# Kernel optimization log

Measured on AMD Instinct MI355X. Metric: run time of the kernel, lower is better.

The kernel has to match this reference:

```python
import jax, jax.numpy as jnp
import numpy as np

D_MODEL = 768
NUM_HEADS = 12
D_K = D_MODEL // NUM_HEADS


def setup_inputs() -> dict:
    key = jax.random.key(0)
    ks = jax.random.split(key, 7)
    B, T = 2, 2048
    scale = 1.0 / np.sqrt(D_MODEL)
    return {
        "query": jax.random.normal(ks[0], (B, T, D_MODEL), dtype=jnp.float32),
        "key": jax.random.normal(ks[1], (B, T, D_MODEL), dtype=jnp.float32),
        "value": jax.random.normal(ks[2], (B, T, D_MODEL), dtype=jnp.float32),
        # nn.Linear(d_model, d_model, bias=False) weights, stored [out, in] as in torch
        "W_q": jax.random.normal(ks[3], (D_MODEL, D_MODEL), dtype=jnp.float32) * scale,
        "W_k": jax.random.normal(ks[4], (D_MODEL, D_MODEL), dtype=jnp.float32) * scale,
        "W_v": jax.random.normal(ks[5], (D_MODEL, D_MODEL), dtype=jnp.float32) * scale,
        "W_o": jax.random.normal(ks[6], (D_MODEL, D_MODEL), dtype=jnp.float32) * scale,
    }


def _split_heads(x):
    # [B, T, H*Dk] -> [B, H, T, Dk]
    B, T, _ = x.shape
    return x.reshape(B, T, NUM_HEADS, D_K).transpose(0, 2, 1, 3)


def reference(query, key, value, W_q, W_k, W_v, W_o):
    # Linear projections (torch Linear: y = x @ W.T)
    Q = _split_heads(query @ W_q.T)
    K = _split_heads(key @ W_k.T)
    V = _split_heads(value @ W_v.T)

    # Naive scaled dot-product attention: full [B,H,Tq,Tk] score matrix
    scores = jnp.einsum("bhqd,bhkd->bhqk", Q, K) / jnp.sqrt(jnp.float32(D_K))
    weights = jax.nn.softmax(scores, axis=-1)
    attn = jnp.einsum("bhqk,bhkd->bhqd", weights, V)

    # [B,H,T,Dk] -> [B,T,D_model], then output projection
    B, H, T, Dk = attn.shape
    attn = attn.transpose(0, 2, 1, 3).reshape(B, T, H * Dk)
    output = attn @ W_o.T
    return output, weights
```

## Files before the change

kernel.cpp:

```cpp
#include <hip/hip_runtime.h>
#include <cstdint>

#define HD   12
#define TSEQ 2048
#define DM   768
#define DK   64
#define BATCH 2
#define NZ   (BATCH * HD)
#define RS_N (NZ * TSEQ)

template<bool SUMA, bool EXPROW>
__device__ __forceinline__ void gemm_nt_core(
    const float* __restrict__ A, const float* __restrict__ A2,
    const float* __restrict__ B, float* __restrict__ C,
    int m0, int n0, int K, int lda, int ldb, int ldc, float alpha,
    float* __restrict__ rowsum, int rowbase)
{
    __shared__ float As[16][132];
    __shared__ float Bs[16][132];

    const int t = threadIdx.x;
    const int row = t & 127;
    const int kh8 = (t >> 7) * 8;
    const float* Arow = A + (size_t)(m0 + row) * lda + kh8;
    const float* Brow = B + (size_t)(n0 + row) * ldb + kh8;
    const float* A2row = nullptr;
    if (SUMA) A2row = A2 + (size_t)(m0 + row) * lda + kh8;

    const int w  = t >> 6;
    const int l  = t & 63;
    const int orow = (w >> 1) * 64 + (l >> 3) * 8;
    const int ocol = (w & 1) * 64 + (l & 7) * 8;

    float acc[8][8];
    #pragma unroll
    for (int i = 0; i < 8; ++i)
        #pragma unroll
        for (int j = 0; j < 8; ++j) acc[i][j] = 0.f;

    float4 a0 = *(const float4*)(Arow);
    float4 a1 = *(const float4*)(Arow + 4);
    float4 b0 = *(const float4*)(Brow);
    float4 b1 = *(const float4*)(Brow + 4);
    float4 c0, c1;
    if (SUMA) { c0 = *(const float4*)(A2row); c1 = *(const float4*)(A2row + 4); }

    for (int k0 = 0; k0 < K; k0 += 16) {
        __syncthreads();
        if (SUMA) {
            a0.x += c0.x; a0.y += c0.y; a0.z += c0.z; a0.w += c0.w;
            a1.x += c1.x; a1.y += c1.y; a1.z += c1.z; a1.w += c1.w;
        }
        As[kh8 + 0][row] = a0.x; As[kh8 + 1][row] = a0.y;
        As[kh8 + 2][row] = a0.z; As[kh8 + 3][row] = a0.w;
        As[kh8 + 4][row] = a1.x; As[kh8 + 5][row] = a1.y;
        As[kh8 + 6][row] = a1.z; As[kh8 + 7][row] = a1.w;
        Bs[kh8 + 0][row] = b0.x; Bs[kh8 + 1][row] = b0.y;
        Bs[kh8 + 2][row] = b0.z; Bs[kh8 + 3][row] = b0.w;
        Bs[kh8 + 4][row] = b1.x; Bs[kh8 + 5][row] = b1.y;
        Bs[kh8 + 6][row] = b1.z; Bs[kh8 + 7][row] = b1.w;
        __syncthreads();
        if (k0 + 16 < K) {
            a0 = *(const float4*)(Arow + k0 + 16);
            a1 = *(const float4*)(Arow + k0 + 20);
            b0 = *(const float4*)(Brow + k0 + 16);
            b1 = *(const float4*)(Brow + k0 + 20);
            if (SUMA) {
                c0 = *(const float4*)(A2row + k0 + 16);
                c1 = *(const float4*)(A2row + k0 + 20);
            }
        }
        #pragma unroll
        for (int kk = 0; kk < 16; ++kk) {
            const float4 f0 = *(const float4*)&As[kk][orow];
            const float4 f1 = *(const float4*)&As[kk][orow + 4];
            const float4 g0 = *(const float4*)&Bs[kk][ocol];
            const float4 g1 = *(const float4*)&Bs[kk][ocol + 4];
            const float a[8] = {f0.x, f0.y, f0.z, f0.w, f1.x, f1.y, f1.z, f1.w};
            const float b[8] = {g0.x, g0.y, g0.z, g0.w, g1.x, g1.y, g1.z, g1.w};
            #pragma unroll
            for (int i = 0; i < 8; ++i)
                #pragma unroll
                for (int j = 0; j < 8; ++j)
                    acc[i][j] = fmaf(a[i], b[j], acc[i][j]);
        }
    }

    if (EXPROW) {
        float rs[8];
        #pragma unroll
        for (int i = 0; i < 8; ++i) {
            rs[i] = 0.f;
            #pragma unroll
            for (int j = 0; j < 8; ++j) {
                acc[i][j] = __expf(acc[i][j] * alpha);
                rs[i] += acc[i][j];
            }
            float* crow = C + (size_t)(m0 + orow + i) * ldc + n0 + ocol;
            *(float4*)crow = make_float4(acc[i][0], acc[i][1], acc[i][2], acc[i][3]);
            *(float4*)(crow + 4) = make_float4(acc[i][4], acc[i][5], acc[i][6], acc[i][7]);
        }
        #pragma unroll
        for (int i = 0; i < 8; ++i) {
            rs[i] += __shfl_xor(rs[i], 1);
            rs[i] += __shfl_xor(rs[i], 2);
            rs[i] += __shfl_xor(rs[i], 4);
        }
        if ((l & 7) == 0) {
            #pragma unroll
            for (int i = 0; i < 8; ++i)
                atomicAdd(&rowsum[rowbase + m0 + orow + i], rs[i]);
        }
    } else {
        #pragma unroll
        for (int i = 0; i < 8; ++i) {
            float* crow = C + (size_t)(m0 + orow + i) * ldc + n0 + ocol;
            *(float4*)crow = make_float4(acc[i][0] * alpha, acc[i][1] * alpha,
                                         acc[i][2] * alpha, acc[i][3] * alpha);
            *(float4*)(crow + 4) = make_float4(acc[i][4] * alpha, acc[i][5] * alpha,
                                               acc[i][6] * alpha, acc[i][7] * alpha);
        }
    }
}

__global__ __launch_bounds__(256) void gemm_qkv(
    const float* __restrict__ q, const float* __restrict__ k,
    const float* __restrict__ v,
    const float* __restrict__ Wq, const float* __restrict__ Wk,
    const float* __restrict__ Wv,
    float* __restrict__ Qp, float* __restrict__ Kp, float* __restrict__ Vp)
{
    const int by  = blockIdx.y;
    const int mat = by / 6;
    const int nb  = by % 6;
    const float* A = (mat == 0) ? q  : (mat == 1) ? k  : v;
    const float* B = (mat == 0) ? Wq : (mat == 1) ? Wk : Wv;
    float*       C = (mat == 0) ? Qp : (mat == 1) ? Kp : Vp;
    gemm_nt_core<false, false>(A, nullptr, B, C, blockIdx.x * 128, nb * 128,
                               DM, DM, DM, DM, 1.f, nullptr, 0);
}

template<bool SUMA>
__global__ __launch_bounds__(256) void gemm_out(
    const float* __restrict__ ctx0, const float* __restrict__ ctx1,
    const float* __restrict__ Wo, float* __restrict__ out)
{
    gemm_nt_core<SUMA, false>(ctx0, ctx1, Wo, out, blockIdx.x * 128,
                              blockIdx.y * 128, DM, DM, DM, DM, 1.f, nullptr, 0);
}

template<bool EXPROW>
__global__ __launch_bounds__(256) void attn_scores(
    const float* __restrict__ Qp, const float* __restrict__ Kp,
    float* __restrict__ Wt, float* __restrict__ rowsum)
{
    const int z = blockIdx.z, b = z / HD, h = z % HD;
    gemm_nt_core<false, EXPROW>(Qp + (size_t)b * TSEQ * DM + h * DK, nullptr,
                                Kp + (size_t)b * TSEQ * DM + h * DK,
                                Wt + (size_t)z * TSEQ * TSEQ,
                                blockIdx.x * 128, blockIdx.y * 128,
                                DK, DM, DM, TSEQ, 0.125f, rowsum, z * TSEQ);
}

__global__ __launch_bounds__(256) void zero_buf(float* __restrict__ p, int n)
{
    const int i = blockIdx.x * 256 + threadIdx.x;
    if (i < n) p[i] = 0.f;
}

__global__ __launch_bounds__(256) void softmax_rows(float* __restrict__ Wt)
{
    float* p = Wt + (size_t)blockIdx.x * TSEQ;
    const int t = threadIdx.x;
    const float4 va = *(const float4*)(p + t * 4);
    const float4 vb = *(const float4*)(p + 1024 + t * 4);
    float v[8] = {va.x, va.y, va.z, va.w, vb.x, vb.y, vb.z, vb.w};

    float m = -3.4e38f;
    #pragma unroll
    for (int i = 0; i < 8; ++i) m = fmaxf(m, v[i]);
    #pragma unroll
    for (int off = 32; off > 0; off >>= 1) m = fmaxf(m, __shfl_down(m, off));
    __shared__ float redm[4];
    __shared__ float reds[4];
    const int lane = t & 63, wid = t >> 6;
    if (lane == 0) redm[wid] = m;
    __syncthreads();
    m = fmaxf(fmaxf(redm[0], redm[1]), fmaxf(redm[2], redm[3]));
    float s = 0.f;
    #pragma unroll
    for (int i = 0; i < 8; ++i) { v[i] = __expf(v[i] - m); s += v[i]; }
    #pragma unroll
    for (int off = 32; off > 0; off >>= 1) s += __shfl_down(s, off);
    if (lane == 0) reds[wid] = s;
    __syncthreads();
    s = reds[0] + reds[1] + reds[2] + reds[3];
    const float inv = 1.f / s;
    *(float4*)(p + t * 4) =
        make_float4(v[0] * inv, v[1] * inv, v[2] * inv, v[3] * inv);
    *(float4*)(p + 1024 + t * 4) =
        make_float4(v[4] * inv, v[5] * inv, v[6] * inv, v[7] * inv);
}

template<bool NORM>
__global__ __launch_bounds__(256) void attn_pv(
    float* __restrict__ Wt, const float* __restrict__ Vp,
    const float* __restrict__ rowsum, float* __restrict__ ctxp, int kchunk)
{
    const int z = blockIdx.z, b = z / HD, h = z % HD;
    const int kbase = blockIdx.y * kchunk;
    float* ctx = ctxp + (size_t)blockIdx.y * (size_t)BATCH * TSEQ * DM;
    float* A = Wt + (size_t)z * TSEQ * TSEQ + kbase;
    const float* V = Vp + ((size_t)b * TSEQ + kbase) * DM + h * DK;

    __shared__ float Ws[16][132];
    __shared__ float Vs[16][68];
    __shared__ float inv_s[128];

    const int t = threadIdx.x;
    const int m0 = blockIdx.x * 128;
    const int arow = t & 127;
    const int kh8  = (t >> 7) * 8;
    float* Arow = A + (size_t)(m0 + arow) * TSEQ + kh8;
    const int vr = t >> 4, vc = (t & 15) * 4;
    const float* Vrow = V + (size_t)vr * DM + vc;
    const int oty = t >> 4;
    const int otx = t & 15;

    if (NORM) {
        if (t < 128) inv_s[t] = 1.f / rowsum[z * TSEQ + m0 + t];
    }
    __syncthreads();
    float winv = 1.f;
    if (NORM) winv = inv_s[arow];

    float acc[8][4];
    #pragma unroll
    for (int i = 0; i < 8; ++i)
        #pragma unroll
        for (int j = 0; j < 4; ++j) acc[i][j] = 0.f;

    float4 a0 = *(const float4*)(Arow);
    float4 a1 = *(const float4*)(Arow + 4);
    float4 vv = *(const float4*)(Vrow);

    for (int k0 = 0; k0 < kchunk; k0 += 16) {
        __syncthreads();
        Ws[kh8 + 0][arow] = a0.x; Ws[kh8 + 1][arow] = a0.y;
        Ws[kh8 + 2][arow] = a0.z; Ws[kh8 + 3][arow] = a0.w;
        Ws[kh8 + 4][arow] = a1.x; Ws[kh8 + 5][arow] = a1.y;
        Ws[kh8 + 6][arow] = a1.z; Ws[kh8 + 7][arow] = a1.w;
        *(float4*)&Vs[vr][vc] = vv;
        __syncthreads();
        if (NORM) {
            *(float4*)(Arow + k0) = make_float4(a0.x * winv, a0.y * winv,
                                                a0.z * winv, a0.w * winv);
            *(float4*)(Arow + k0 + 4) = make_float4(a1.x * winv, a1.y * winv,
                                                    a1.z * winv, a1.w * winv);
        }
        if (k0 + 16 < kchunk) {
            a0 = *(const float4*)(Arow + k0 + 16);
            a1 = *(const float4*)(Arow + k0 + 20);
            vv = *(const float4*)(Vrow + (size_t)(k0 + 16) * DM);
        }
        #pragma unroll
        for (int kk = 0; kk < 16; ++kk) {
            const float4 a0v = *(const float4*)&Ws[kk][oty * 8];
            const float4 a1v = *(const float4*)&Ws[kk][oty * 8 + 4];
            const float4 bv  = *(const float4*)&Vs[kk][otx * 4];
            const float a[8] = {a0v.x, a0v.y, a0v.z, a0v.w,
                                a1v.x, a1v.y, a1v.z, a1v.w};
            const float bb[4] = {bv.x, bv.y, bv.z, bv.w};
            #pragma unroll
            for (int i = 0; i < 8; ++i)
                #pragma unroll
                for (int j = 0; j < 4; ++j)
                    acc[i][j] = fmaf(a[i], bb[j], acc[i][j]);
        }
    }

    float* cbase = ctx + ((size_t)b * TSEQ + m0 + oty * 8) * DM + h * DK + otx * 4;
    #pragma unroll
    for (int i = 0; i < 8; ++i) {
        float s = 1.f;
        if (NORM) s = inv_s[oty * 8 + i];
        *(float4*)(cbase + (size_t)i * DM) =
            make_float4(acc[i][0] * s, acc[i][1] * s, acc[i][2] * s, acc[i][3] * s);
    }
}

extern "C" void kernel_launch(void* const* d_in, const int* in_sizes, int n_in,
                              void* d_out, int out_size, void* d_ws, size_t ws_size,
                              hipStream_t stream)
{
    const float* q  = (const float*)d_in[0];
    const float* k  = (const float*)d_in[1];
    const float* v  = (const float*)d_in[2];
    const float* Wq = (const float*)d_in[3];
    const float* Wk = (const float*)d_in[4];
    const float* Wv = (const float*)d_in[5];
    const float* Wo = (const float*)d_in[6];

    float* out = (float*)d_out;
    const int BT = BATCH * TSEQ;
    float* wts = out + (size_t)BT * DM;

    const size_t bufE = (size_t)BT * DM;
    float* Qp   = (float*)d_ws;
    float* Kp   = Qp + bufE;
    float* Vp   = Kp + bufE;
    float* ctx0 = Vp + bufE;
    float* ctx1 = ctx0 + bufE;

    const bool fit2 = ws_size >= (5 * bufE + RS_N) * sizeof(float);
    const bool fit1 = ws_size >= (4 * bufE + RS_N) * sizeof(float);

    gemm_qkv<<<dim3(BT / 128, 18), 256, 0, stream>>>(q, k, v, Wq, Wk, Wv,
                                                     Qp, Kp, Vp);

    if (fit1) {
        const int nsplit = fit2 ? 2 : 1;
        float* rowsum = (fit2 ? ctx1 + bufE : ctx0 + bufE);
        zero_buf<<<RS_N / 256, 256, 0, stream>>>(rowsum, RS_N);
        attn_scores<true><<<dim3(TSEQ / 128, TSEQ / 128, NZ), 256, 0, stream>>>(
            Qp, Kp, wts, rowsum);
        attn_pv<true><<<dim3(TSEQ / 128, nsplit, NZ), 256, 0, stream>>>(
            wts, Vp, rowsum, ctx0, TSEQ / nsplit);
        if (nsplit == 2)
            gemm_out<true><<<dim3(BT / 128, DM / 128), 256, 0, stream>>>(
                ctx0, ctx1, Wo, out);
        else
            gemm_out<false><<<dim3(BT / 128, DM / 128), 256, 0, stream>>>(
                ctx0, nullptr, Wo, out);
    } else {
        attn_scores<false><<<dim3(TSEQ / 128, TSEQ / 128, NZ), 256, 0, stream>>>(
            Qp, Kp, wts, nullptr);
        softmax_rows<<<NZ * TSEQ, 256, 0, stream>>>(wts);
        attn_pv<false><<<dim3(TSEQ / 128, 1, NZ), 256, 0, stream>>>(
            wts, Vp, nullptr, ctx0, TSEQ);
        gemm_out<false><<<dim3(BT / 128, DM / 128), 256, 0, stream>>>(
            ctx0, nullptr, Wo, out);
    }
}
```

Measured before the change: 1.211 ms.

## Replace global rowsum atomics with per-tile partial sums and allow 4-way PV split

Row sums of the exponentiated scores are now reduced in shared memory per tile and written to a per-key-tile partial buffer, rather than accumulated with global atomics into a buffer that had to be zeroed first. The zeroing kernel is gone, and the PV kernel sums the partials itself. The PV stage can also split the key dimension four ways when the workspace is large enough, and the output GEMM sums four context buffers. The cost is more workspace, extra reads of the context buffers in the output projection, and two extra block barriers in the score epilogue.

```diff
diff --git a/kernel.cpp b/kernel.cpp
--- a/kernel.cpp
+++ b/kernel.cpp
@@ -7,14 +7,16 @@
 #define DK   64
 #define BATCH 2
 #define NZ   (BATCH * HD)
-#define RS_N (NZ * TSEQ)
-
-template<bool SUMA, bool EXPROW>
+#define KT   (TSEQ / 128)
+#define PS_N ((size_t)NZ * KT * TSEQ)
+
+template<int NSUM, bool EXPROW>
 __device__ __forceinline__ void gemm_nt_core(
     const float* __restrict__ A, const float* __restrict__ A2,
+    const float* __restrict__ A3, const float* __restrict__ A4,
     const float* __restrict__ B, float* __restrict__ C,
     int m0, int n0, int K, int lda, int ldb, int ldc, float alpha,
-    float* __restrict__ rowsum, int rowbase)
+    float* __restrict__ rowsum_slice)
 {
     __shared__ float As[16][132];
     __shared__ float Bs[16][132];
@@ -24,8 +26,9 @@
     const int kh8 = (t >> 7) * 8;
     const float* Arow = A + (size_t)(m0 + row) * lda + kh8;
     const float* Brow = B + (size_t)(n0 + row) * ldb + kh8;
-    const float* A2row = nullptr;
-    if (SUMA) A2row = A2 + (size_t)(m0 + row) * lda + kh8;
+    const float* A2row = (NSUM >= 2) ? (A2 + (size_t)(m0 + row) * lda + kh8) : nullptr;
+    const float* A3row = (NSUM >= 4) ? (A3 + (size_t)(m0 + row) * lda + kh8) : nullptr;
+    const float* A4row = (NSUM >= 4) ? (A4 + (size_t)(m0 + row) * lda + kh8) : nullptr;
 
     const int w  = t >> 6;
     const int l  = t & 63;
@@ -42,14 +45,24 @@
     float4 a1 = *(const float4*)(Arow + 4);
     float4 b0 = *(const float4*)(Brow);
     float4 b1 = *(const float4*)(Brow + 4);
-    float4 c0, c1;
-    if (SUMA) { c0 = *(const float4*)(A2row); c1 = *(const float4*)(A2row + 4); }
+    float4 c20, c21, c30, c31, c40, c41;
+    if (NSUM >= 2) { c20 = *(const float4*)(A2row); c21 = *(const float4*)(A2row + 4); }
+    if (NSUM >= 4) {
+        c30 = *(const float4*)(A3row); c31 = *(const float4*)(A3row + 4);
+        c40 = *(const float4*)(A4row); c41 = *(const float4*)(A4row + 4);
+    }
 
     for (int k0 = 0; k0 < K; k0 += 16) {
         __syncthreads();
-        if (SUMA) {
-            a0.x += c0.x; a0.y += c0.y; a0.z += c0.z; a0.w += c0.w;
-            a1.x += c1.x; a1.y += c1.y; a1.z += c1.z; a1.w += c1.w;
+        if (NSUM >= 2) {
+            a0.x += c20.x; a0.y += c20.y; a0.z += c20.z; a0.w += c20.w;
+            a1.x += c21.x; a1.y += c21.y; a1.z += c21.z; a1.w += c21.w;
+        }
+        if (NSUM >= 4) {
+            a0.x += c30.x + c40.x; a0.y += c30.y + c40.y;
+            a0.z += c30.z + c40.z; a0.w += c30.w + c40.w;
+            a1.x += c31.x + c41.x; a1.y += c31.y + c41.y;
+            a1.z += c31.z + c41.z; a1.w += c31.w + c41.w;
         }
         As[kh8 + 0][row] = a0.x; As[kh8 + 1][row] = a0.y;
         As[kh8 + 2][row] = a0.z; As[kh8 + 3][row] = a0.w;
@@ -65,9 +78,15 @@
             a1 = *(const float4*)(Arow + k0 + 20);
             b0 = *(const float4*)(Brow + k0 + 16);
             b1 = *(const float4*)(Brow + k0 + 20);
-            if (SUMA) {
-                c0 = *(const float4*)(A2row + k0 + 16);
-                c1 = *(const float4*)(A2row + k0 + 20);
+            if (NSUM >= 2) {
+                c20 = *(const float4*)(A2row + k0 + 16);
+                c21 = *(const float4*)(A2row + k0 + 20);
+            }
+            if (NSUM >= 4) {
+                c30 = *(const float4*)(A3row + k0 + 16);
+                c31 = *(const float4*)(A3row + k0 + 20);
+                c40 = *(const float4*)(A4row + k0 + 16);
+                c41 = *(const float4*)(A4row + k0 + 20);
             }
         }
         #pragma unroll
@@ -106,11 +125,16 @@
             rs[i] += __shfl_xor(rs[i], 2);
             rs[i] += __shfl_xor(rs[i], 4);
         }
+        __shared__ float part[128];
+        if (t < 128) part[t] = 0.f;
+        __syncthreads();
         if ((l & 7) == 0) {
             #pragma unroll
             for (int i = 0; i < 8; ++i)
-                atomicAdd(&rowsum[rowbase + m0 + orow + i], rs[i]);
-        }
+                atomicAdd(&part[orow + i], rs[i]);
+        }
+        __syncthreads();
+        if (t < 128) rowsum_slice[m0 + t] = part[t];
     } else {
         #pragma unroll
         for (int i = 0; i < 8; ++i) {
@@ -136,36 +160,36 @@
     const float* A = (mat == 0) ? q  : (mat == 1) ? k  : v;
     const float* B = (mat == 0) ? Wq : (mat == 1) ? Wk : Wv;
     float*       C = (mat == 0) ? Qp : (mat == 1) ? Kp : Vp;
-    gemm_nt_core<false, false>(A, nullptr, B, C, blockIdx.x * 128, nb * 128,
-                               DM, DM, DM, DM, 1.f, nullptr, 0);
-}
-
-template<bool SUMA>
+    gemm_nt_core<1, false>(A, nullptr, nullptr, nullptr, B, C,
+                           blockIdx.x * 128, nb * 128, DM, DM, DM, DM, 1.f,
+                           nullptr);
+}
+
+template<int NSUM>
 __global__ __launch_bounds__(256) void gemm_out(
-    const float* __restrict__ ctx0, const float* __restrict__ ctx1,
+    const float* __restrict__ c0, const float* __restrict__ c1,
+    const float* __restrict__ c2, const float* __restrict__ c3,
     const float* __restrict__ Wo, float* __restrict__ out)
 {
-    gemm_nt_core<SUMA, false>(ctx0, ctx1, Wo, out, blockIdx.x * 128,
-                              blockIdx.y * 128, DM, DM, DM, DM, 1.f, nullptr, 0);
+    gemm_nt_core<NSUM, false>(c0, c1, c2, c3, Wo, out,
+                              blockIdx.x * 128, blockIdx.y * 128,
+                              DM, DM, DM, DM, 1.f, nullptr);
 }
 
 template<bool EXPROW>
 __global__ __launch_bounds__(256) void attn_scores(
     const float* __restrict__ Qp, const float* __restrict__ Kp,
-    float* __restrict__ Wt, float* __restrict__ rowsum)
+    float* __restrict__ Wt, float* __restrict__ rowsum_p)
 {
     const int z = blockIdx.z, b = z / HD, h = z % HD;
-    gemm_nt_core<false, EXPROW>(Qp + (size_t)b * TSEQ * DM + h * DK, nullptr,
-                                Kp + (size_t)b * TSEQ * DM + h * DK,
-                                Wt + (size_t)z * TSEQ * TSEQ,
-                                blockIdx.x * 128, blockIdx.y * 128,
-                                DK, DM, DM, TSEQ, 0.125f, rowsum, z * TSEQ);
-}
-
-__global__ __launch_bounds__(256) void zero_buf(float* __restrict__ p, int n)
-{
-    const int i = blockIdx.x * 256 + threadIdx.x;
-    if (i < n) p[i] = 0.f;
+    float* slice = EXPROW
+        ? rowsum_p + ((size_t)z * KT + blockIdx.y) * TSEQ : nullptr;
+    gemm_nt_core<1, EXPROW>(Qp + (size_t)b * TSEQ * DM + h * DK,
+                            nullptr, nullptr, nullptr,
+                            Kp + (size_t)b * TSEQ * DM + h * DK,
+                            Wt + (size_t)z * TSEQ * TSEQ,
+                            blockIdx.x * 128, blockIdx.y * 128,
+                            DK, DM, DM, TSEQ, 0.125f, slice);
 }
 
 __global__ __launch_bounds__(256) void softmax_rows(float* __restrict__ Wt)
@@ -205,7 +229,7 @@
 template<bool NORM>
 __global__ __launch_bounds__(256) void attn_pv(
     float* __restrict__ Wt, const float* __restrict__ Vp,
-    const float* __restrict__ rowsum, float* __restrict__ ctxp, int kchunk)
+    const float* __restrict__ rowsum_p, float* __restrict__ ctxp, int kchunk)
 {
     const int z = blockIdx.z, b = z / HD, h = z % HD;
     const int kbase = blockIdx.y * kchunk;
@@ -228,11 +252,16 @@
     const int otx = t & 15;
 
     if (NORM) {
-        if (t < 128) inv_s[t] = 1.f / rowsum[z * TSEQ + m0 + t];
-    }
-    __syncthreads();
-    float winv = 1.f;
-    if (NORM) winv = inv_s[arow];
+        if (t < 128) {
+            float s = 0.f;
+            const float* rp = rowsum_p + (size_t)z * KT * TSEQ + m0 + t;
+            #pragma unroll
+            for (int j = 0; j < KT; ++j) s += rp[(size_t)j * TSEQ];
+            inv_s[t] = 1.f / s;
+        }
+        __syncthreads();
+    }
+    const float winv = NORM ? inv_s[arow] : 1.f;
 
     float acc[8][4];
     #pragma unroll
@@ -282,8 +311,7 @@
     float* cbase = ctx + ((size_t)b * TSEQ + m0 + oty * 8) * DM + h * DK + otx * 4;
     #pragma unroll
     for (int i = 0; i < 8; ++i) {
-        float s = 1.f;
-        if (NORM) s = inv_s[oty * 8 + i];
+        const float s = NORM ? inv_s[oty * 8 + i] : 1.f;
         *(float4*)(cbase + (size_t)i * DM) =
             make_float4(acc[i][0] * s, acc[i][1] * s, acc[i][2] * s, acc[i][3] * s);
     }
@@ -310,35 +338,40 @@
     float* Kp   = Qp + bufE;
     float* Vp   = Kp + bufE;
     float* ctx0 = Vp + bufE;
-    float* ctx1 = ctx0 + bufE;
-
-    const bool fit2 = ws_size >= (5 * bufE + RS_N) * sizeof(float);
-    const bool fit1 = ws_size >= (4 * bufE + RS_N) * sizeof(float);
+
+    const int nsplit =
+        (ws_size >= (7 * bufE + PS_N) * sizeof(float)) ? 4 :
+        (ws_size >= (5 * bufE + PS_N) * sizeof(float)) ? 2 :
+        (ws_size >= (4 * bufE + PS_N) * sizeof(float)) ? 1 : 0;
 
     gemm_qkv<<<dim3(BT / 128, 18), 256, 0, stream>>>(q, k, v, Wq, Wk, Wv,
                                                      Qp, Kp, Vp);
 
-    if (fit1) {
-        const int nsplit = fit2 ? 2 : 1;
-        float* rowsum = (fit2 ? ctx1 + bufE : ctx0 + bufE);
-        zero_buf<<<RS_N / 256, 256, 0, stream>>>(rowsum, RS_N);
+    if (nsplit > 0) {
+        float* rowsum_p = ctx0 + (size_t)nsplit * bufE;
         attn_scores<true><<<dim3(TSEQ / 128, TSEQ / 128, NZ), 256, 0, stream>>>(
-            Qp, Kp, wts, rowsum);
+            Qp, Kp, wts, rowsum_p);
         attn_pv<true><<<dim3(TSEQ / 128, nsplit, NZ), 256, 0, stream>>>(
-            wts, Vp, rowsum, ctx0, TSEQ / nsplit);
-        if (nsplit == 2)
-            gemm_out<true><<<dim3(BT / 128, DM / 128), 256, 0, stream>>>(
-                ctx0, ctx1, Wo, out);
+            wts, Vp, rowsum_p, ctx0, TSEQ / nsplit);
+        float* c1 = ctx0 + bufE;
+        float* c2 = c1 + bufE;
+        float* c3 = c2 + bufE;
+        if (nsplit == 4)
+            gemm_out<4><<<dim3(BT / 128, DM / 128), 256, 0, stream>>>(
+                ctx0, c1, c2, c3, Wo, out);
+        else if (nsplit == 2)
+            gemm_out<2><<<dim3(BT / 128, DM / 128), 256, 0, stream>>>(
+                ctx0, c1, nullptr, nullptr, Wo, out);
         else
-            gemm_out<false><<<dim3(BT / 128, DM / 128), 256, 0, stream>>>(
-                ctx0, nullptr, Wo, out);
+            gemm_out<1><<<dim3(BT / 128, DM / 128), 256, 0, stream>>>(
+                ctx0, nullptr, nullptr, nullptr, Wo, out);
     } else {
         attn_scores<false><<<dim3(TSEQ / 128, TSEQ / 128, NZ), 256, 0, stream>>>(
             Qp, Kp, wts, nullptr);
         softmax_rows<<<NZ * TSEQ, 256, 0, stream>>>(wts);
         attn_pv<false><<<dim3(TSEQ / 128, 1, NZ), 256, 0, stream>>>(
             wts, Vp, nullptr, ctx0, TSEQ);
-        gemm_out<false><<<dim3(BT / 128, DM / 128), 256, 0, stream>>>(
-            ctx0, nullptr, Wo, out);
-    }
-}
+        gemm_out<1><<<dim3(BT / 128, DM / 128), 256, 0, stream>>>(
+            ctx0, nullptr, nullptr, nullptr, Wo, out);
+    }
+}
```

New measurement: 1.150 ms. -5.1%, faster.
